# Performance work log

Hardware: AMD Instinct MI355X
Metric: run time of the kernel (lower is better)

Reference implementation:

```python
import jax, jax.numpy as jnp
import numpy as np

N = 50000       # nodes
E = 800000      # edges
IN = 256        # input channels
H = 4           # heads
C = 64          # hidden channels per head
NEG_SLOPE = 0.2 # PyG GATConv default LeakyReLU slope
EPS = 1e-16


def setup_inputs() -> dict:
    key = jax.random.key(0)
    k_x, k_e, k_w, k_as, k_ad = jax.random.split(key, 5)
    x = jax.random.normal(k_x, (N, IN), dtype=jnp.float32)
    edge_index = jax.random.randint(k_e, (2, E), 0, N, dtype=jnp.int64)
    # GATConv params: glorot-style scale
    W = jax.random.normal(k_w, (IN, H * C), dtype=jnp.float32) * (1.0 / np.sqrt(IN))
    att_src = jax.random.normal(k_as, (H, C), dtype=jnp.float32) * (1.0 / np.sqrt(C))
    att_dst = jax.random.normal(k_ad, (H, C), dtype=jnp.float32) * (1.0 / np.sqrt(C))
    return {"x": x, "edge_index": edge_index, "W": W, "att_src": att_src, "att_dst": att_dst}


def reference(x, edge_index, W, att_src, att_dst):
    src, dst = edge_index[0], edge_index[1]
    # linear projection, split heads: [N, H, C]
    xh = (x @ W).reshape(N, H, C)
    # per-node attention halves: [N, H]
    a_src = jnp.einsum('nhc,hc->nh', xh, att_src)
    a_dst = jnp.einsum('nhc,hc->nh', xh, att_dst)
    # per-edge logits with LeakyReLU: [E, H]
    alpha = a_src[src] + a_dst[dst]
    alpha = jnp.where(alpha >= 0, alpha, NEG_SLOPE * alpha)
    # segment softmax over destination nodes
    m = jax.ops.segment_max(alpha, dst, num_segments=N)          # [N, H]
    ex = jnp.exp(alpha - m[dst])                                  # [E, H]
    denom = jax.ops.segment_sum(ex, dst, num_segments=N)         # [N, H]
    att = ex / (denom[dst] + EPS)                                 # [E, H]
    # weighted message scatter-add: [N, H, C] -> concat heads [N, H*C]
    msg = att[:, :, None] * xh[src]                               # [E, H, C]
    out = jax.ops.segment_sum(msg, dst, num_segments=N)
    out = out.reshape(N, H * C)
    return (out, att)
```

## Files before the change

kernel.cpp:

```cpp
#include <hip/hip_runtime.h>
#include <math.h>

#define IN_CH   256
#define HC      256
#define H_HEADS 4
#define NEG_SLOPE 0.2f

typedef __attribute__((ext_vector_type(8))) short short8;
typedef __attribute__((ext_vector_type(4))) short short4v;
typedef __attribute__((ext_vector_type(4))) float float4v;

__device__ __forceinline__ float bf2f(unsigned short b) {
    return __uint_as_float(((unsigned)b) << 16);
}
__device__ __forceinline__ unsigned short f2bf(float f) {
    unsigned u = __float_as_uint(f);
    u += 0x7fffu + ((u >> 16) & 1u);
    return (unsigned short)(u >> 16);
}
__device__ __forceinline__ float lrelu(float a) {
    return a >= 0.f ? a : NEG_SLOPE * a;
}


__global__ void prep_w(const float* __restrict__ w,
                       unsigned short* __restrict__ wt) {
    int idx = blockIdx.x * 256 + threadIdx.x;
    int k = idx >> 8, c = idx & 255;
    wt[(size_t)c * 256 + k] = f2bf(w[idx]);
}

__global__ __launch_bounds__(256) void prep_x(const float* __restrict__ x,
                                              unsigned short* __restrict__ x_hi,
                                              unsigned short* __restrict__ x_lo,
                                              int total4) {
    int i = blockIdx.x * 256 + threadIdx.x;
    if (i >= total4) return;
    float4v v = ((const float4v*)x)[i];
    short4v hi, lo;
#pragma unroll
    for (int j = 0; j < 4; ++j) {
        unsigned short h = f2bf(v[j]);
        hi[j] = (short)h;
        lo[j] = (short)f2bf(v[j] - bf2f(h));
    }
    ((short4v*)x_hi)[i] = hi;
    ((short4v*)x_lo)[i] = lo;
}

__global__ __launch_bounds__(256) void gemm_xh(const unsigned short* __restrict__ x_hi,
                                               const unsigned short* __restrict__ x_lo,
                                               const unsigned short* __restrict__ wt,
                                               const float* __restrict__ att_s,
                                               const float* __restrict__ att_d,
                                               unsigned short* __restrict__ xh_bf,
                                               float* __restrict__ a_src,
                                               float* __restrict__ a_dst, int N) {
    __shared__ __attribute__((aligned(16))) unsigned char lds_a[16384];
    int tid  = threadIdx.x;
    int wave = tid >> 6;
    int lane = tid & 63;
    int quad = lane >> 4;
    int l16  = lane & 15;
    int rb   = blockIdx.x * 16;

#pragma unroll
    for (int pass = 0; pass < 4; ++pass) {
        int q    = pass * 256 + tid;
        int half = q >> 9;
        int s    = q & 511;
        int kc   = s >> 4;
        int m    = s & 15;
        int grow = rb + m; if (grow >= N) grow = N - 1;
        const unsigned short* gp =
            (half ? x_lo : x_hi) + (size_t)grow * IN_CH + kc * 8;
        short8 v = *(const short8*)gp;
        *(short8*)(lds_a + (size_t)q * 16) = v;
    }
    __syncthreads();

    float4v acc[4] = {};
    const unsigned short* wt_base = wt + ((size_t)wave * 64 + l16) * IN_CH;
#pragma unroll
    for (int k0 = 0; k0 < 8; ++k0) {
        int kc   = k0 * 4 + quad;
        int slot = kc * 16 + l16;
        short8 a_hi = *(const short8*)(lds_a + slot * 16);
        short8 a_lo = *(const short8*)(lds_a + 8192 + slot * 16);
#pragma unroll
        for (int ct = 0; ct < 4; ++ct) {
            short8 bh = *(const short8*)(wt_base + (size_t)ct * 16 * IN_CH
                                         + k0 * 32 + quad * 8);
            acc[ct] = __builtin_amdgcn_mfma_f32_16x16x32_bf16(a_lo, bh, acc[ct], 0, 0, 0);
            acc[ct] = __builtin_amdgcn_mfma_f32_16x16x32_bf16(a_hi, bh, acc[ct], 0, 0, 0);
        }
    }

    int cb = wave;
    float ps[4] = {0.f, 0.f, 0.f, 0.f};
    float pd[4] = {0.f, 0.f, 0.f, 0.f};
#pragma unroll
    for (int ct = 0; ct < 4; ++ct) {
        float as_c = att_s[cb * 64 + ct * 16 + l16];
        float ad_c = att_d[cb * 64 + ct * 16 + l16];
#pragma unroll
        for (int r = 0; r < 4; ++r) {
            float v = acc[ct][r];
            int grow = rb + quad * 4 + r;
            if (grow < N)
                xh_bf[(size_t)grow * HC + cb * 64 + ct * 16 + l16] = f2bf(v);
            ps[r] += v * as_c;
            pd[r] += v * ad_c;
        }
    }
#pragma unroll
    for (int off = 1; off < 16; off <<= 1) {
#pragma unroll
        for (int r = 0; r < 4; ++r) {
            ps[r] += __shfl_xor(ps[r], off);
            pd[r] += __shfl_xor(pd[r], off);
        }
    }
    if (l16 == 0) {
#pragma unroll
        for (int r = 0; r < 4; ++r) {
            int grow = rb + quad * 4 + r;
            if (grow < N) {
                a_src[(size_t)grow * 4 + cb] = ps[r];
                a_dst[(size_t)grow * 4 + cb] = pd[r];
            }
        }
    }
}

__global__ __launch_bounds__(256) void deg_count(const int* __restrict__ ei,
                                                 int* __restrict__ deg, int E) {
    int e = blockIdx.x * 256 + threadIdx.x;
    if (e >= E) return;
    atomicAdd(deg + ei[E + e], 1);
}


__global__ __launch_bounds__(256) void scan_part(const int* __restrict__ deg,
                                                 int* __restrict__ part, int N) {
    int t = threadIdx.x;
    int base = blockIdx.x * 1024 + t * 4;
    int s = 0;
    if (base + 4 <= N) {
        int4 v = *(const int4*)(deg + base);
        s = v.x + v.y + v.z + v.w;
    } else {
#pragma unroll
        for (int j = 0; j < 4; ++j)
            if (base + j < N) s += deg[base + j];
    }
#pragma unroll
    for (int off = 1; off < 64; off <<= 1) s += __shfl_xor(s, off);
    __shared__ int ws[4];
    if ((t & 63) == 0) ws[t >> 6] = s;
    __syncthreads();
    if (t == 0) part[blockIdx.x] = ws[0] + ws[1] + ws[2] + ws[3];
}

__global__ __launch_bounds__(1024) void scan_mid(int* __restrict__ part, int NB) {
    __shared__ int sm[1024];
    int t = threadIdx.x;
    int v = (t < NB) ? part[t] : 0;
    sm[t] = v;
    __syncthreads();
    for (int off = 1; off < 1024; off <<= 1) {
        int tmp = (t >= off) ? sm[t - off] : 0;
        __syncthreads();
        sm[t] += tmp;
        __syncthreads();
    }
    if (t < NB) part[t] = sm[t] - v;
}

__global__ __launch_bounds__(256) void scan_final(const int* __restrict__ deg,
                                                  const int* __restrict__ part,
                                                  int* __restrict__ rowptr,
                                                  int* __restrict__ cursor, int N) {
    __shared__ int sm[256];
    int t = threadIdx.x;
    int base = blockIdx.x * 1024 + t * 4;
    int v0 = 0, v1 = 0, v2 = 0, v3 = 0;
    if (base + 4 <= N) {
        int4 v = *(const int4*)(deg + base);
        v0 = v.x; v1 = v.y; v2 = v.z; v3 = v.w;
    } else {
        if (base + 0 < N) v0 = deg[base + 0];
        if (base + 1 < N) v1 = deg[base + 1];
        if (base + 2 < N) v2 = deg[base + 2];
        if (base + 3 < N) v3 = deg[base + 3];
    }
    int s = v0 + v1 + v2 + v3;
    sm[t] = s;
    __syncthreads();
    for (int off = 1; off < 256; off <<= 1) {
        int tmp = (t >= off) ? sm[t - off] : 0;
        __syncthreads();
        sm[t] += tmp;
        __syncthreads();
    }
    int run = part[blockIdx.x] + sm[t] - s;
    int r0 = run, r1 = r0 + v0, r2 = r1 + v1, r3 = r2 + v2;
    if (base + 4 <= N) {
        *(int4*)(rowptr + base) = (int4){r0, r1, r2, r3};
        *(int4*)(cursor + base) = (int4){r0, r1, r2, r3};
    } else {
        if (base + 0 < N) { rowptr[base + 0] = r0; cursor[base + 0] = r0; }
        if (base + 1 < N) { rowptr[base + 1] = r1; cursor[base + 1] = r1; }
        if (base + 2 < N) { rowptr[base + 2] = r2; cursor[base + 2] = r2; }
        if (base + 3 < N) { rowptr[base + 3] = r3; cursor[base + 3] = r3; }
    }
}

__global__ __launch_bounds__(256) void fill_csr(const int* __restrict__ ei,
                                                int* __restrict__ cursor,
                                                int* __restrict__ csr_src, int E) {
    int e = blockIdx.x * 256 + threadIdx.x;
    if (e >= E) return;
    int s = ei[e], d = ei[E + e];
    int slot = atomicAdd(cursor + d, 1);
    csr_src[slot] = s;
}

__global__ __launch_bounds__(256) void gat_gather(const int* __restrict__ csr_src,
                                                  const int* __restrict__ rowptr,
                                                  const int* __restrict__ deg,
                                                  const float* __restrict__ a_src,
                                                  const float* __restrict__ a_dst,
                                                  const unsigned short* __restrict__ xh_bf,
                                                  float* __restrict__ out,
                                                  float* __restrict__ pack, int N) {
    int wave = threadIdx.x >> 6, lane = threadIdx.x & 63;
    int d = blockIdx.x * 4 + wave;
    if (d >= N) return;
    int h = lane >> 4;
    int start = rowptr[d], cnt = deg[d];
    float adst = a_dst[(size_t)d * 4 + h];

    if (cnt == 0) {
        *(float4v*)(out + (size_t)d * HC + lane * 4) = (float4v){0.f, 0.f, 0.f, 0.f};
        if ((lane & 15) == 0) {
            pack[(size_t)d * 12 + h]     = adst;
            pack[(size_t)d * 12 + 4 + h] = 0.f;
            pack[(size_t)d * 12 + 8 + h] = 0.f;
        }
        return;
    }

    float mE = -INFINITY, lE = 0.f, mO = -INFINITY, lO = 0.f;
    float4v accE = {0.f, 0.f, 0.f, 0.f}, accO = {0.f, 0.f, 0.f, 0.f};

    int s2 = 0, s3 = 0;
    float asE = 0.f, asO = 0.f;
    short4v xvE = {}, xvO = {};
    {
        int s0 = csr_src[start];
        asE = a_src[(size_t)s0 * 4 + h];
        xvE = *(const short4v*)(xh_bf + (size_t)s0 * HC + lane * 4);
    }
    if (cnt > 1) {
        int s1 = csr_src[start + 1];
        asO = a_src[(size_t)s1 * 4 + h];
        xvO = *(const short4v*)(xh_bf + (size_t)s1 * HC + lane * 4);
    }
    if (cnt > 2) s2 = csr_src[start + 2];
    if (cnt > 3) s3 = csr_src[start + 3];

    for (int i = 0; i < cnt; i += 2) {
        float asE_n = 0.f, asO_n = 0.f;
        short4v xvE_n = {}, xvO_n = {};
        if (i + 2 < cnt) {
            asE_n = a_src[(size_t)s2 * 4 + h];
            xvE_n = *(const short4v*)(xh_bf + (size_t)s2 * HC + lane * 4);
        }
        if (i + 3 < cnt) {
            asO_n = a_src[(size_t)s3 * 4 + h];
            xvO_n = *(const short4v*)(xh_bf + (size_t)s3 * HC + lane * 4);
        }
        int s4 = (i + 4 < cnt) ? csr_src[start + i + 4] : 0;
        int s5 = (i + 5 < cnt) ? csr_src[start + i + 5] : 0;
        {
            float al = lrelu(asE + adst);
            float mn = fmaxf(mE, al);
            float sc = __expf(mE - mn);
            float p  = __expf(al - mn);
            lE = lE * sc + p;
#pragma unroll
            for (int j = 0; j < 4; ++j)
                accE[j] = accE[j] * sc + p * bf2f((unsigned short)xvE[j]);
            mE = mn;
        }
        if (i + 1 < cnt) {
            float al = lrelu(asO + adst);
            float mn = fmaxf(mO, al);
            float sc = __expf(mO - mn);
            float p  = __expf(al - mn);
            lO = lO * sc + p;
#pragma unroll
            for (int j = 0; j < 4; ++j)
                accO[j] = accO[j] * sc + p * bf2f((unsigned short)xvO[j]);
            mO = mn;
        }
        asE = asE_n; xvE = xvE_n; asO = asO_n; xvO = xvO_n;
        s2 = s4; s3 = s5;
    }
    float mm = fmaxf(mE, mO);
    float sE = __expf(mE - mm), sO = __expf(mO - mm);
    float l  = lE * sE + lO * sO;
    float inv = 1.f / (l + 1e-16f);
    float4v o;
#pragma unroll
    for (int j = 0; j < 4; ++j) o[j] = (accE[j] * sE + accO[j] * sO) * inv;
    *(float4v*)(out + (size_t)d * HC + lane * 4) = o;
    if ((lane & 15) == 0) {
        pack[(size_t)d * 12 + h]     = adst;
        pack[(size_t)d * 12 + 4 + h] = mm;
        pack[(size_t)d * 12 + 8 + h] = inv;
    }
}

__global__ __launch_bounds__(256) void att_edge(const int* __restrict__ ei,
                                                const float* __restrict__ a_src,
                                                const float* __restrict__ pack,
                                                float* __restrict__ att_out, int E) {
    int e = blockIdx.x * 256 + threadIdx.x;
    if (e >= E) return;
    int s = ei[e], d = ei[E + e];
    float4v as = *(const float4v*)(a_src + (size_t)s * 4);
    float4v ad = *(const float4v*)(pack + (size_t)d * 12);
    float4v mm = *(const float4v*)(pack + (size_t)d * 12 + 4);
    float4v gg = *(const float4v*)(pack + (size_t)d * 12 + 8);
    float4v o;
#pragma unroll
    for (int h = 0; h < 4; ++h)
        o[h] = __expf(lrelu(as[h] + ad[h]) - mm[h]) * gg[h];
    *(float4v*)(att_out + (size_t)e * 4) = o;
}

extern "C" void kernel_launch(void* const* d_in, const int* in_sizes, int n_in,
                              void* d_out, int out_size, void* d_ws, size_t ws_size,
                              hipStream_t stream) {
    const float* x     = (const float*)d_in[0];
    const int*   ei    = (const int*)d_in[1];
    const float* W     = (const float*)d_in[2];
    const float* att_s = (const float*)d_in[3];
    const float* att_d = (const float*)d_in[4];

    const int N = in_sizes[0] / IN_CH;
    const int E = in_sizes[1] / 2;

    char* ws = (char*)d_ws;
    size_t off = 0;
    unsigned short* xh_bf = (unsigned short*)(ws + off); off += (size_t)N * HC * 2;
    unsigned short* x_hi  = (unsigned short*)(ws + off); off += (size_t)N * IN_CH * 2;
    unsigned short* x_lo  = (unsigned short*)(ws + off); off += (size_t)N * IN_CH * 2;
    unsigned short* wt    = (unsigned short*)(ws + off); off += (size_t)IN_CH * HC * 2;
    float* a_src = (float*)(ws + off); off += (size_t)N * H_HEADS * 4;
    float* a_dst = (float*)(ws + off); off += (size_t)N * H_HEADS * 4;
    float* pack  = (float*)(ws + off); off += (size_t)N * 12 * 4;
    int* rowptr  = (int*)(ws + off); off += (size_t)N * 4;
    int* cursor  = (int*)(ws + off); off += (size_t)N * 4;
    int* csr_src = (int*)(ws + off); off += (size_t)E * 4;
    int* part    = (int*)(ws + off); off += 1024 * 4;
    size_t zoff = off;
    int* deg     = (int*)(ws + off); off += (size_t)N * 4;

    float* out     = (float*)d_out;
    float* out_att = out + (size_t)N * HC;

    hipMemsetAsync(ws + zoff, 0, off - zoff, stream);

    const int NB = (N + 1023) / 1024;

    prep_w<<<256, 256, 0, stream>>>(W, wt);
    prep_x<<<(N * IN_CH / 4 + 255) / 256, 256, 0, stream>>>(x, x_hi, x_lo, N * IN_CH / 4);
    deg_count<<<(E + 255) / 256, 256, 0, stream>>>(ei, deg, E);
    gemm_xh<<<(N + 15) / 16, 256, 0, stream>>>(x_hi, x_lo, wt, att_s, att_d,
                                               xh_bf, a_src, a_dst, N);
    scan_part<<<NB, 256, 0, stream>>>(deg, part, N);
    scan_mid<<<1, 1024, 0, stream>>>(part, NB);
    scan_final<<<NB, 256, 0, stream>>>(deg, part, rowptr, cursor, N);
    fill_csr<<<(E + 255) / 256, 256, 0, stream>>>(ei, cursor, csr_src, E);
    gat_gather<<<(N + 3) / 4, 256, 0, stream>>>(csr_src, rowptr, deg, a_src, a_dst,
                                                xh_bf, out, pack, N);
    att_edge<<<(E + 255) / 256, 256, 0, stream>>>(ei, a_src, pack, out_att, E);
}
```

Baseline: 347.8 us.

## Fuse x split into GEMM, drop scan_mid, use exp2 and deferred rescale softmax

The fp32-to-bf16 hi/lo split of x now happens inside the GEMM's LDS load, so the prep_x kernel and its intermediate buffers are gone. scan_mid is removed; each scan_final block sums the preceding block partials itself. Attention logits are pre-scaled by log2(e) so every exp becomes a hardware exp2. The online softmax in the gather skips the running-max rescale when all lanes' logits stay within a threshold of the current max. This cuts x memory traffic, one launch and exp/rescale work, but the deferred rescale allows partial sums to grow by up to 2^12 before renormalising.

```diff
diff --git a/kernel.cpp b/kernel.cpp
--- a/kernel.cpp
+++ b/kernel.cpp
@@ -5,6 +5,8 @@
 #define HC      256
 #define H_HEADS 4
 #define NEG_SLOPE 0.2f
+#define LOG2E   1.44269504088896f
+#define DEFER_THR 12.0f
 
 typedef __attribute__((ext_vector_type(8))) short short8;
 typedef __attribute__((ext_vector_type(4))) short short4v;
@@ -20,6 +22,9 @@
 }
 __device__ __forceinline__ float lrelu(float a) {
     return a >= 0.f ? a : NEG_SLOPE * a;
+}
+__device__ __forceinline__ float fexp2(float a) {
+    return __builtin_amdgcn_exp2f(a);
 }
 
 
@@ -30,26 +35,7 @@
     wt[(size_t)c * 256 + k] = f2bf(w[idx]);
 }
 
-__global__ __launch_bounds__(256) void prep_x(const float* __restrict__ x,
-                                              unsigned short* __restrict__ x_hi,
-                                              unsigned short* __restrict__ x_lo,
-                                              int total4) {
-    int i = blockIdx.x * 256 + threadIdx.x;
-    if (i >= total4) return;
-    float4v v = ((const float4v*)x)[i];
-    short4v hi, lo;
-#pragma unroll
-    for (int j = 0; j < 4; ++j) {
-        unsigned short h = f2bf(v[j]);
-        hi[j] = (short)h;
-        lo[j] = (short)f2bf(v[j] - bf2f(h));
-    }
-    ((short4v*)x_hi)[i] = hi;
-    ((short4v*)x_lo)[i] = lo;
-}
-
-__global__ __launch_bounds__(256) void gemm_xh(const unsigned short* __restrict__ x_hi,
-                                               const unsigned short* __restrict__ x_lo,
+__global__ __launch_bounds__(256) void gemm_xh(const float* __restrict__ x,
                                                const unsigned short* __restrict__ wt,
                                                const float* __restrict__ att_s,
                                                const float* __restrict__ att_d,
@@ -65,17 +51,26 @@
     int rb   = blockIdx.x * 16;
 
 #pragma unroll
-    for (int pass = 0; pass < 4; ++pass) {
-        int q    = pass * 256 + tid;
-        int half = q >> 9;
-        int s    = q & 511;
-        int kc   = s >> 4;
-        int m    = s & 15;
+    for (int pass = 0; pass < 2; ++pass) {
+        int s  = pass * 256 + tid;
+        int kc = s >> 4;
+        int m  = s & 15;
         int grow = rb + m; if (grow >= N) grow = N - 1;
-        const unsigned short* gp =
-            (half ? x_lo : x_hi) + (size_t)grow * IN_CH + kc * 8;
-        short8 v = *(const short8*)gp;
-        *(short8*)(lds_a + (size_t)q * 16) = v;
+        const float* gp = x + (size_t)grow * IN_CH + kc * 8;
+        float4v f0 = *(const float4v*)gp;
+        float4v f1 = *(const float4v*)(gp + 4);
+        short8 hi, lo;
+#pragma unroll
+        for (int j = 0; j < 4; ++j) {
+            unsigned short h0 = f2bf(f0[j]);
+            hi[j] = (short)h0;
+            lo[j] = (short)f2bf(f0[j] - bf2f(h0));
+            unsigned short h1 = f2bf(f1[j]);
+            hi[4 + j] = (short)h1;
+            lo[4 + j] = (short)f2bf(f1[j] - bf2f(h1));
+        }
+        *(short8*)(lds_a + (size_t)s * 16) = hi;
+        *(short8*)(lds_a + 8192 + (size_t)s * 16) = lo;
     }
     __syncthreads();
 
@@ -101,8 +96,8 @@
     float pd[4] = {0.f, 0.f, 0.f, 0.f};
 #pragma unroll
     for (int ct = 0; ct < 4; ++ct) {
-        float as_c = att_s[cb * 64 + ct * 16 + l16];
-        float ad_c = att_d[cb * 64 + ct * 16 + l16];
+        float as_c = att_s[cb * 64 + ct * 16 + l16] * LOG2E;
+        float ad_c = att_d[cb * 64 + ct * 16 + l16] * LOG2E;
 #pragma unroll
         for (int r = 0; r < 4; ++r) {
             float v = acc[ct][r];
@@ -162,27 +157,19 @@
     if (t == 0) part[blockIdx.x] = ws[0] + ws[1] + ws[2] + ws[3];
 }
 
-__global__ __launch_bounds__(1024) void scan_mid(int* __restrict__ part, int NB) {
-    __shared__ int sm[1024];
-    int t = threadIdx.x;
-    int v = (t < NB) ? part[t] : 0;
-    sm[t] = v;
-    __syncthreads();
-    for (int off = 1; off < 1024; off <<= 1) {
-        int tmp = (t >= off) ? sm[t - off] : 0;
-        __syncthreads();
-        sm[t] += tmp;
-        __syncthreads();
-    }
-    if (t < NB) part[t] = sm[t] - v;
-}
-
 __global__ __launch_bounds__(256) void scan_final(const int* __restrict__ deg,
                                                   const int* __restrict__ part,
                                                   int* __restrict__ rowptr,
                                                   int* __restrict__ cursor, int N) {
     __shared__ int sm[256];
+    __shared__ int wsum[4];
     int t = threadIdx.x;
+    int bacc = 0;
+    for (int j = t; j < blockIdx.x; j += 256) bacc += part[j];
+#pragma unroll
+    for (int off = 1; off < 64; off <<= 1) bacc += __shfl_xor(bacc, off);
+    if ((t & 63) == 0) wsum[t >> 6] = bacc;
+
     int base = blockIdx.x * 1024 + t * 4;
     int v0 = 0, v1 = 0, v2 = 0, v3 = 0;
     if (base + 4 <= N) {
@@ -203,7 +190,8 @@
         sm[t] += tmp;
         __syncthreads();
     }
-    int run = part[blockIdx.x] + sm[t] - s;
+    int boff = wsum[0] + wsum[1] + wsum[2] + wsum[3];
+    int run = boff + sm[t] - s;
     int r0 = run, r1 = r0 + v0, r2 = r1 + v1, r3 = r2 + v2;
     if (base + 4 <= N) {
         *(int4*)(rowptr + base) = (int4){r0, r1, r2, r3};
@@ -283,33 +271,55 @@
         }
         int s4 = (i + 4 < cnt) ? csr_src[start + i + 4] : 0;
         int s5 = (i + 5 < cnt) ? csr_src[start + i + 5] : 0;
-        {
-            float al = lrelu(asE + adst);
-            float mn = fmaxf(mE, al);
-            float sc = __expf(mE - mn);
-            float p  = __expf(al - mn);
-            lE = lE * sc + p;
+
+        bool haveO = (i + 1 < cnt);
+        float alE = lrelu(asE + adst);
+        bool ok = (alE <= mE + DEFER_THR);
+        float alO = 0.f;
+        if (haveO) {
+            alO = lrelu(asO + adst);
+            ok = ok && (alO <= mO + DEFER_THR);
+        }
+        if (__all(ok)) {
+            float p = fexp2(alE - mE);
+            lE += p;
 #pragma unroll
             for (int j = 0; j < 4; ++j)
-                accE[j] = accE[j] * sc + p * bf2f((unsigned short)xvE[j]);
-            mE = mn;
-        }
-        if (i + 1 < cnt) {
-            float al = lrelu(asO + adst);
-            float mn = fmaxf(mO, al);
-            float sc = __expf(mO - mn);
-            float p  = __expf(al - mn);
-            lO = lO * sc + p;
-#pragma unroll
-            for (int j = 0; j < 4; ++j)
-                accO[j] = accO[j] * sc + p * bf2f((unsigned short)xvO[j]);
-            mO = mn;
+                accE[j] += p * bf2f((unsigned short)xvE[j]);
+            if (haveO) {
+                float q = fexp2(alO - mO);
+                lO += q;
+#pragma unroll
+                for (int j = 0; j < 4; ++j)
+                    accO[j] += q * bf2f((unsigned short)xvO[j]);
+            }
+        } else {
+            {
+                float mn = fmaxf(mE, alE);
+                float sc = fexp2(mE - mn);
+                float p  = fexp2(alE - mn);
+                lE = lE * sc + p;
+#pragma unroll
+                for (int j = 0; j < 4; ++j)
+                    accE[j] = accE[j] * sc + p * bf2f((unsigned short)xvE[j]);
+                mE = mn;
+            }
+            if (haveO) {
+                float mn = fmaxf(mO, alO);
+                float sc = fexp2(mO - mn);
+                float p  = fexp2(alO - mn);
+                lO = lO * sc + p;
+#pragma unroll
+                for (int j = 0; j < 4; ++j)
+                    accO[j] = accO[j] * sc + p * bf2f((unsigned short)xvO[j]);
+                mO = mn;
+            }
         }
         asE = asE_n; xvE = xvE_n; asO = asO_n; xvO = xvO_n;
         s2 = s4; s3 = s5;
     }
     float mm = fmaxf(mE, mO);
-    float sE = __expf(mE - mm), sO = __expf(mO - mm);
+    float sE = fexp2(mE - mm), sO = fexp2(mO - mm);
     float l  = lE * sE + lO * sO;
     float inv = 1.f / (l + 1e-16f);
     float4v o;
@@ -337,7 +347,7 @@
     float4v o;
 #pragma unroll
     for (int h = 0; h < 4; ++h)
-        o[h] = __expf(lrelu(as[h] + ad[h]) - mm[h]) * gg[h];
+        o[h] = fexp2(lrelu(as[h] + ad[h]) - mm[h]) * gg[h];
     *(float4v*)(att_out + (size_t)e * 4) = o;
 }
 
@@ -356,8 +366,6 @@
     char* ws = (char*)d_ws;
     size_t off = 0;
     unsigned short* xh_bf = (unsigned short*)(ws + off); off += (size_t)N * HC * 2;
-    unsigned short* x_hi  = (unsigned short*)(ws + off); off += (size_t)N * IN_CH * 2;
-    unsigned short* x_lo  = (unsigned short*)(ws + off); off += (size_t)N * IN_CH * 2;
     unsigned short* wt    = (unsigned short*)(ws + off); off += (size_t)IN_CH * HC * 2;
     float* a_src = (float*)(ws + off); off += (size_t)N * H_HEADS * 4;
     float* a_dst = (float*)(ws + off); off += (size_t)N * H_HEADS * 4;
@@ -372,17 +380,15 @@
     float* out     = (float*)d_out;
     float* out_att = out + (size_t)N * HC;
 
-    hipMemsetAsync(ws + zoff, 0, off - zoff, stream);
+    (void)hipMemsetAsync(ws + zoff, 0, off - zoff, stream);
 
     const int NB = (N + 1023) / 1024;
 
     prep_w<<<256, 256, 0, stream>>>(W, wt);
-    prep_x<<<(N * IN_CH / 4 + 255) / 256, 256, 0, stream>>>(x, x_hi, x_lo, N * IN_CH / 4);
     deg_count<<<(E + 255) / 256, 256, 0, stream>>>(ei, deg, E);
-    gemm_xh<<<(N + 15) / 16, 256, 0, stream>>>(x_hi, x_lo, wt, att_s, att_d,
+    gemm_xh<<<(N + 15) / 16, 256, 0, stream>>>(x, wt, att_s, att_d,
                                                xh_bf, a_src, a_dst, N);
     scan_part<<<NB, 256, 0, stream>>>(deg, part, N);
-    scan_mid<<<1, 1024, 0, stream>>>(part, NB);
     scan_final<<<NB, 256, 0, stream>>>(deg, part, rowptr, cursor, N);
     fill_csr<<<(E + 255) / 256, 256, 0, stream>>>(ei, cursor, csr_src, E);
     gat_gather<<<(N + 3) / 4, 256, 0, stream>>>(csr_src, rowptr, deg, a_src, a_dst,
```

Result: faster. 332.1 us (-4.5%).
